# Kernel optimization log

Measured on AMD Instinct MI355X. Metric: run time of the kernel, lower is better.

The kernel has to match this reference:

```python
import jax, jax.numpy as jnp
import numpy as np

B, N, D = 4, 4096, 1024
H, S, R = 16, 256, 2           # heads, segment size, dilation rate
DH = D // H
LN_EPS = 1e-5


def _hilbert_perm(n_side):
    # perm[d] = linear index (y*side + x) of the d-th point on the Hilbert curve
    def d2xy(n, d):
        x = y = 0
        t = d
        s = 1
        while s < n:
            rx = 1 & (t // 2)
            ry = 1 & (t ^ rx)
            if ry == 0:
                if rx == 1:
                    x = s - 1 - x
                    y = s - 1 - y
                x, y = y, x
            x += s * rx
            y += s * ry
            t //= 4
            s *= 2
        return x, y
    perm = np.empty(n_side * n_side, dtype=np.int32)
    for d in range(n_side * n_side):
        xx, yy = d2xy(n_side, d)
        perm[d] = yy * n_side + xx
    return perm


def setup_inputs() -> dict:
    key = jax.random.key(0)
    ks = jax.random.split(key, 8)
    sc = 0.02
    return {
        "x": jax.random.normal(ks[0], (B, N, D), jnp.float32),
        "ln1_g": jnp.ones((D,), jnp.float32),
        "ln1_b": jnp.zeros((D,), jnp.float32),
        "w_qkv": jax.random.normal(ks[1], (D, 3 * D), jnp.float32) * sc,
        "b_qkv": jnp.zeros((3 * D,), jnp.float32),
        "w_o": jax.random.normal(ks[2], (D, D), jnp.float32) * sc,
        "b_o": jnp.zeros((D,), jnp.float32),
        "ln2_g": jnp.ones((D,), jnp.float32),
        "ln2_b": jnp.zeros((D,), jnp.float32),
        "w1": jax.random.normal(ks[3], (D, 4 * D), jnp.float32) * sc,
        "b1": jnp.zeros((4 * D,), jnp.float32),
        "w2": jax.random.normal(ks[4], (4 * D, D), jnp.float32) * sc,
        "b2": jnp.zeros((D,), jnp.float32),
        "hilbert_perm": jnp.asarray(_hilbert_perm(int(np.sqrt(N)))),
    }


def _layernorm(x, g, b):
    mu = jnp.mean(x, axis=-1, keepdims=True)
    var = jnp.mean(jnp.square(x - mu), axis=-1, keepdims=True)
    return (x - mu) * jax.lax.rsqrt(var + LN_EPS) * g + b


def _hilbert_dilated_attention(x, w_qkv, b_qkv, w_o, b_o, perm):
    b, n, d = x.shape
    nseg, sr = n // S, S // R
    xp = jnp.take(x, perm, axis=1)                    # Hilbert reorder
    qkv = xp @ w_qkv + b_qkv                          # [b,n,3d]
    q, k, v = jnp.split(qkv, 3, axis=-1)
    def seg(t):
        return t.reshape(b, nseg, S, H, DH)
    q, k, v = seg(q), seg(k), seg(v)
    # per-head dilation offset: head h attends positions (h % R) :: R in each segment
    offs = jnp.arange(H, dtype=jnp.int32) % R                        # [H]
    idx = offs[None, :] + R * jnp.arange(sr, dtype=jnp.int32)[:, None]  # [sr,H]
    idx_g = idx[None, None, :, :, None]                              # [1,1,sr,H,1]
    qd = jnp.take_along_axis(q, idx_g, axis=2)        # [b,nseg,sr,H,dh]
    kd = jnp.take_along_axis(k, idx_g, axis=2)
    vd = jnp.take_along_axis(v, idx_g, axis=2)
    scores = jnp.einsum('bgqhd,bgkhd->bghqk', qd, kd) / jnp.sqrt(jnp.asarray(DH, x.dtype))
    attn = jax.nn.softmax(scores, axis=-1)
    od = jnp.einsum('bghqk,bgkhd->bgqhd', attn, vd)   # [b,nseg,sr,H,dh]
    # scatter back into full segments; uncovered (head,pos) slots stay zero
    out = jnp.zeros((b, nseg, S, H, DH), x.dtype)
    out = out.at[:, :, idx, jnp.arange(H)[None, :], :].set(od)
    out = out.reshape(b, n, d) @ w_o + b_o
    inv = jnp.argsort(perm)
    return jnp.take(out, inv, axis=1)                 # inverse Hilbert reorder


def reference(x, ln1_g, ln1_b, w_qkv, b_qkv, w_o, b_o, ln2_g, ln2_b, w1, b1, w2, b2, hilbert_perm):
    h = _layernorm(x, ln1_g, ln1_b)
    h = _hilbert_dilated_attention(h, w_qkv, b_qkv, w_o, b_o, hilbert_perm)
    x = x + h
    h = _layernorm(x, ln2_g, ln2_b)
    h = jax.nn.gelu(h @ w1 + b1, approximate=False) @ w2 + b2
    return x + h
```

## Files before the change

kernel.cpp:

```cpp
#include <hip/hip_runtime.h>

typedef short bf16x8 __attribute__((ext_vector_type(8)));
typedef float f32x4 __attribute__((ext_vector_type(4)));
typedef unsigned short u16;

#define GLDS16(g, l) __builtin_amdgcn_global_load_lds( \
    (const __attribute__((address_space(1))) void*)(g), \
    (__attribute__((address_space(3))) void*)(l), 16, 0, 0)

__device__ __forceinline__ u16 f2b(float f) {
  unsigned u = __float_as_uint(f);
  u += 0x7fffu + ((u >> 16) & 1u);
  return (u16)(u >> 16);
}

__global__ __launch_bounds__(256)
void transpose_bf16(const float* __restrict__ w, u16* __restrict__ wt, int K, int N) {
  __shared__ float tile[32][33];
  const int n0 = blockIdx.x * 32, k0 = blockIdx.y * 32;
  const int tx = threadIdx.x & 31, ty = threadIdx.x >> 5;
#pragma unroll
  for (int i = 0; i < 4; ++i)
    tile[ty + i * 8][tx] = w[(size_t)(k0 + ty + i * 8) * N + n0 + tx];
  __syncthreads();
#pragma unroll
  for (int i = 0; i < 4; ++i)
    wt[(size_t)(n0 + ty + i * 8) * K + k0 + tx] = f2b(tile[tx][ty + i * 8]);
}

__global__ __launch_bounds__(256)
void ln_rows(const float* __restrict__ src, const float* __restrict__ gam,
             const float* __restrict__ bet, const int* __restrict__ perm,
             u16* __restrict__ dst) {
  const int orow = blockIdx.x;
  const int b = orow >> 12, j = orow & 4095;
  const int srow = perm ? ((b << 12) + perm[j]) : orow;
  const float4 v = ((const float4*)(src + (size_t)srow * 1024))[threadIdx.x];
  float s = v.x + v.y + v.z + v.w;
  float s2 = v.x * v.x + v.y * v.y + v.z * v.z + v.w * v.w;
#pragma unroll
  for (int d = 1; d < 64; d <<= 1) { s += __shfl_xor(s, d); s2 += __shfl_xor(s2, d); }
  __shared__ float rs[4], rs2[4];
  const int wave = threadIdx.x >> 6, lane = threadIdx.x & 63;
  if (lane == 0) { rs[wave] = s; rs2[wave] = s2; }
  __syncthreads();
  s = rs[0] + rs[1] + rs[2] + rs[3];
  s2 = rs2[0] + rs2[1] + rs2[2] + rs2[3];
  const float mu = s * (1.f / 1024.f);
  const float var = s2 * (1.f / 1024.f) - mu * mu;
  const float rstd = rsqrtf(var + 1e-5f);
  const int c = threadIdx.x * 4;
  const float4 gg = *(const float4*)(gam + c);
  const float4 bb = *(const float4*)(bet + c);
  const u16 o0 = f2b((v.x - mu) * rstd * gg.x + bb.x);
  const u16 o1 = f2b((v.y - mu) * rstd * gg.y + bb.y);
  const u16 o2 = f2b((v.z - mu) * rstd * gg.z + bb.z);
  const u16 o3 = f2b((v.w - mu) * rstd * gg.w + bb.w);
  const unsigned lo = (unsigned)o0 | ((unsigned)o1 << 16);
  const unsigned hi = (unsigned)o2 | ((unsigned)o3 << 16);
  *(uint2*)(dst + (size_t)orow * 1024 + c) = make_uint2(lo, hi);
}

template <int EPI>
__global__ __launch_bounds__(512, 2)
void gemm256(const u16* __restrict__ A, const u16* __restrict__ Bt,
             const float* __restrict__ bias, void* __restrict__ Cout,
             const float* __restrict__ resid, const int* __restrict__ perm,
             int M, int Nn, int K) {
  __shared__ u16 sm[65536];
  char* const smc = (char*)sm;
  const int tid = threadIdx.x;
  const int w = tid >> 6, lane = tid & 63;
  const int lr = lane & 15, lg = lane >> 4;
  const int wm = w >> 2, wn = w & 3;

  int wg = blockIdx.x;
  const int nwg = gridDim.x;
  if ((nwg & 7) == 0) { const int per = nwg >> 3; wg = (wg & 7) * per + (wg >> 3); }
  const int gx = M >> 8;
  const int m0 = (wg % gx) << 8, n0 = (wg / gx) << 8;

  const int srow = tid >> 3;
  const int scol = ((tid & 7) ^ (srow & 7)) << 3;
  const size_t aSrc = (size_t)(m0 + srow) * K + scol;
  const size_t bSrc = (size_t)(n0 + srow) * K + scol;
  char* const lWav = smc + w * 1024;

  const int slot0 = (lg ^ (lr & 7)) << 4;
  const int aRow = (wm * 128 + lr) * 128;
  const int bRow = (wn * 64 + lr) * 128 + 32768;

  const int NT = K >> 6;

#define STAGE_(d, mat, h, k0) do { \
    const u16* gp = ((mat) ? Bt : A) + ((mat) ? bSrc : aSrc) + (size_t)(h) * 128 * K + (k0); \
    char* lp = lWav + (d) * 65536 + (mat) * 32768 + (h) * 16384; \
    GLDS16(gp, lp); GLDS16(gp + (size_t)64 * K, lp + 8192); } while (0)

#define BAR_() do { asm volatile("" ::: "memory"); __builtin_amdgcn_s_barrier(); \
                    asm volatile("" ::: "memory"); } while (0)

  bf16x8 aLo[8], aHi[8], bb[8];

#define R_ALO(P) do { _Pragma("unroll") for (int mf = 0; mf < 4; ++mf) \
    _Pragma("unroll") for (int kk = 0; kk < 2; ++kk) \
      aLo[mf * 2 + kk] = *(const bf16x8*)((P) + mf * 2048 + (slot0 ^ (kk << 6))); } while (0)
#define R_AHI(P) do { _Pragma("unroll") for (int mf = 0; mf < 4; ++mf) \
    _Pragma("unroll") for (int kk = 0; kk < 2; ++kk) \
      aHi[mf * 2 + kk] = *(const bf16x8*)((P) + (4 + mf) * 2048 + (slot0 ^ (kk << 6))); } while (0)
#define R_B01(P) do { _Pragma("unroll") for (int nf = 0; nf < 2; ++nf) \
    _Pragma("unroll") for (int kk = 0; kk < 2; ++kk) \
      bb[nf * 2 + kk] = *(const bf16x8*)((P) + nf * 2048 + (slot0 ^ (kk << 6))); } while (0)
#define R_B23(P) do { _Pragma("unroll") for (int nf = 0; nf < 2; ++nf) \
    _Pragma("unroll") for (int kk = 0; kk < 2; ++kk) \
      bb[4 + nf * 2 + kk] = *(const bf16x8*)((P) + (2 + nf) * 2048 + (slot0 ^ (kk << 6))); } while (0)

#define C_QUAD(AARR, NB, MB) do { _Pragma("unroll") for (int mf = 0; mf < 4; ++mf) \
    _Pragma("unroll") for (int nf = 0; nf < 2; ++nf) \
    _Pragma("unroll") for (int kk = 0; kk < 2; ++kk) \
      acc[(MB) * 4 + mf][(NB) * 2 + nf] = __builtin_amdgcn_mfma_f32_16x16x32_bf16( \
          AARR[mf * 2 + kk], bb[(NB) * 4 + nf * 2 + kk], acc[(MB) * 4 + mf][(NB) * 2 + nf], 0, 0, 0); } while (0)

  STAGE_(0, 1, 0, 0); STAGE_(0, 1, 1, 0); STAGE_(0, 0, 0, 0); STAGE_(0, 0, 1, 0);
  if (NT > 1) {
    STAGE_(1, 1, 0, 64); STAGE_(1, 1, 1, 64); STAGE_(1, 0, 0, 64);
    asm volatile("s_waitcnt vmcnt(6)" ::: "memory");
  } else {
    asm volatile("s_waitcnt vmcnt(0)" ::: "memory");
  }
  BAR_();

  f32x4 acc[8][4] = {};
  R_ALO(smc + aRow);
  R_B01(smc + bRow);

  for (int t = 0; t < NT; ++t) {
    const int c = t & 1;
    const char* cA = smc + c * 65536 + aRow;
    const char* cB = smc + c * 65536 + bRow;
    const char* nA = smc + (c ^ 1) * 65536 + aRow;
    const char* nB = smc + (c ^ 1) * 65536 + bRow;

    R_B23(cB);
    if (t + 1 < NT) STAGE_(c ^ 1, 0, 1, (t + 1) << 6);
    BAR_();
    __builtin_amdgcn_s_setprio(1);
    C_QUAD(aLo, 0, 0);
    __builtin_amdgcn_s_setprio(0);
    BAR_();

    R_AHI(cA);
    if (t + 2 < NT) STAGE_(c, 1, 0, (t + 2) << 6);
    BAR_();
    __builtin_amdgcn_s_setprio(1);
    C_QUAD(aLo, 1, 0);
    __builtin_amdgcn_s_setprio(0);
    BAR_();

    if (t + 2 < NT) STAGE_(c, 1, 1, (t + 2) << 6);
    BAR_();
    __builtin_amdgcn_s_setprio(1);
    C_QUAD(aHi, 0, 1);
    __builtin_amdgcn_s_setprio(0);
    BAR_();

    if (t + 2 < NT) STAGE_(c, 0, 0, (t + 2) << 6);
    if (t < NT - 2) asm volatile("s_waitcnt vmcnt(6)" ::: "memory");
    else            asm volatile("s_waitcnt vmcnt(0)" ::: "memory");
    BAR_();
    if (t + 1 < NT) { R_ALO(nA); R_B01(nB); }
    __builtin_amdgcn_s_setprio(1);
    C_QUAD(aHi, 1, 1);
    __builtin_amdgcn_s_setprio(0);
    BAR_();
  }
#undef STAGE_
#undef BAR_
#undef R_ALO
#undef R_AHI
#undef R_B01
#undef R_B23
#undef C_QUAD

#pragma unroll
  for (int mf = 0; mf < 8; ++mf) {
#pragma unroll
    for (int nf = 0; nf < 4; ++nf) {
      const int col = n0 + wn * 64 + nf * 16 + lr;
      const float bia = bias[col];
#pragma unroll
      for (int r = 0; r < 4; ++r) {
        const int row = m0 + wm * 128 + mf * 16 + lg * 4 + r;
        float v = acc[mf][nf][r] + bia;
        if (EPI == 0) {
          ((u16*)Cout)[(size_t)row * Nn + col] = f2b(v);
        } else if (EPI == 1) {
          v = 0.5f * v * (1.f + erff(v * 0.70710678118654752f));
          ((u16*)Cout)[(size_t)row * Nn + col] = f2b(v);
        } else if (EPI == 2) {
          const int b = row >> 12, j = row & 4095;
          const size_t di = ((size_t)((b << 12) + perm[j])) * 1024 + col;
          ((float*)Cout)[di] = resid[di] + v;
        } else {
          const size_t di = (size_t)row * 1024 + col;
          ((float*)Cout)[di] = resid[di] + v;
        }
      }
    }
  }
}

__global__ __launch_bounds__(256, 2)
void attn_kernel(const u16* __restrict__ qkv, u16* __restrict__ outp) {
  const int blk = blockIdx.x;
  const int h = blk & 15, g = (blk >> 4) & 15, b = blk >> 8;
  const int tid = threadIdx.x, wave = tid >> 6, lane = tid & 63;
  const int lr = lane & 15, lg = lane >> 4;
  const int par = h & 1;

  __shared__ u16 lQ[128 * 64];
  __shared__ u16 lK[128 * 64];
  __shared__ u16 lVt[64 * 128];
  __shared__ u16 lP[4][32 * 128];

  const size_t rbase = (size_t)((b << 12) + (g << 8) + par);

#pragma unroll
  for (int i = 0; i < 4; ++i) {
    const int ou = i * 4096 + wave * 1024;
    const int o = ou + lane * 16;
    const int j = o >> 7, cb = o & 127;
    const u16* gq = qkv + (rbase + 2 * j) * 3072 + h * 64 + (cb >> 1);
    GLDS16(gq, (char*)lQ + ou);
    GLDS16(gq + 1024, (char*)lK + ou);
  }
#pragma unroll
  for (int i = 0; i < 4; ++i) {
    const int c = tid + i * 256;
    const int j = c >> 3, dc = c & 7;
    const uint4 vv = *(const uint4*)(qkv + (rbase + 2 * j) * 3072 + 2048 + h * 64 + dc * 8);
    const u16* pv = (const u16*)&vv;
#pragma unroll
    for (int e = 0; e < 8; ++e) lVt[(dc * 8 + e) * 128 + j] = pv[e];
  }
  __syncthreads();

  f32x4 sacc[2][8] = {};
#pragma unroll
  for (int kk = 0; kk < 2; ++kk) {
    bf16x8 aq[2], bk[8];
#pragma unroll
    for (int mf = 0; mf < 2; ++mf)
      aq[mf] = *(const bf16x8*)&lQ[(wave * 32 + mf * 16 + lr) * 64 + kk * 32 + lg * 8];
#pragma unroll
    for (int nf = 0; nf < 8; ++nf)
      bk[nf] = *(const bf16x8*)&lK[(nf * 16 + lr) * 64 + kk * 32 + lg * 8];
#pragma unroll
    for (int mf = 0; mf < 2; ++mf)
#pragma unroll
      for (int nf = 0; nf < 8; ++nf)
        sacc[mf][nf] = __builtin_amdgcn_mfma_f32_16x16x32_bf16(aq[mf], bk[nf], sacc[mf][nf], 0, 0, 0);
  }

#pragma unroll
  for (int mf = 0; mf < 2; ++mf) {
#pragma unroll
    for (int r = 0; r < 4; ++r) {
      float mx = -3e38f;
#pragma unroll
      for (int nf = 0; nf < 8; ++nf) mx = fmaxf(mx, sacc[mf][nf][r]);
#pragma unroll
      for (int d = 1; d < 16; d <<= 1) mx = fmaxf(mx, __shfl_xor(mx, d));
      float pv[8];
      float sum = 0.f;
#pragma unroll
      for (int nf = 0; nf < 8; ++nf) {
        pv[nf] = __expf((sacc[mf][nf][r] - mx) * 0.125f);
        sum += pv[nf];
      }
#pragma unroll
      for (int d = 1; d < 16; d <<= 1) sum += __shfl_xor(sum, d);
      const float inv = 1.f / sum;
      const int rrow = mf * 16 + lg * 4 + r;
#pragma unroll
      for (int nf = 0; nf < 8; ++nf)
        lP[wave][rrow * 128 + nf * 16 + lr] = f2b(pv[nf] * inv);
    }
  }
  __syncthreads();

  f32x4 oacc[2][4] = {};
#pragma unroll
  for (int kk = 0; kk < 4; ++kk) {
    bf16x8 ap[2], bv[4];
#pragma unroll
    for (int mf = 0; mf < 2; ++mf)
      ap[mf] = *(const bf16x8*)&lP[wave][(mf * 16 + lr) * 128 + kk * 32 + lg * 8];
#pragma unroll
    for (int nf = 0; nf < 4; ++nf)
      bv[nf] = *(const bf16x8*)&lVt[(nf * 16 + lr) * 128 + kk * 32 + lg * 8];
#pragma unroll
    for (int mf = 0; mf < 2; ++mf)
#pragma unroll
      for (int nf = 0; nf < 4; ++nf)
        oacc[mf][nf] = __builtin_amdgcn_mfma_f32_16x16x32_bf16(ap[mf], bv[nf], oacc[mf][nf], 0, 0, 0);
  }

  u16* obase = outp + ((size_t)((b << 12) + (g << 8))) * 1024 + h * 64;
#pragma unroll
  for (int mf = 0; mf < 2; ++mf)
#pragma unroll
    for (int nf = 0; nf < 4; ++nf)
#pragma unroll
      for (int r = 0; r < 4; ++r) {
        const int jq = wave * 32 + mf * 16 + lg * 4 + r;
        obase[(size_t)(par + 2 * jq) * 1024 + nf * 16 + lr] = f2b(oacc[mf][nf][r]);
      }
  const int jz = tid >> 1, hh = (tid & 1) * 32;
  u16* zp = obase + (size_t)((1 - par) + 2 * jz) * 1024 + hh;
  const uint4 z = make_uint4(0u, 0u, 0u, 0u);
#pragma unroll
  for (int i = 0; i < 4; ++i) ((uint4*)zp)[i] = z;
}

extern "C" void kernel_launch(void* const* d_in, const int* in_sizes, int n_in,
                              void* d_out, int out_size, void* d_ws, size_t ws_size,
                              hipStream_t stream) {
  const float* x    = (const float*)d_in[0];
  const float* ln1g = (const float*)d_in[1];
  const float* ln1b = (const float*)d_in[2];
  const float* wqkv = (const float*)d_in[3];
  const float* bqkv = (const float*)d_in[4];
  const float* wo   = (const float*)d_in[5];
  const float* bo   = (const float*)d_in[6];
  const float* ln2g = (const float*)d_in[7];
  const float* ln2b = (const float*)d_in[8];
  const float* w1   = (const float*)d_in[9];
  const float* b1   = (const float*)d_in[10];
  const float* w2   = (const float*)d_in[11];
  const float* b2   = (const float*)d_in[12];
  const int*   perm = (const int*)d_in[13];
  float* out = (float*)d_out;
  char* ws = (char*)d_ws;

  u16*  r0    = (u16*)ws;
  u16*  qkv   = (u16*)(ws + (32ull << 20));
  u16*  a1    = (u16*)(ws + (32ull << 20));
  float* x2   = (float*)(ws + (160ull << 20));
  u16*  wqkvT = (u16*)(ws + (224ull << 20));
  u16*  woT   = (u16*)(ws + (230ull << 20));
  u16*  w1T   = (u16*)(ws + (232ull << 20));
  u16*  w2T   = (u16*)(ws + (240ull << 20));

  transpose_bf16<<<dim3(3072 / 32, 1024 / 32), 256, 0, stream>>>(wqkv, wqkvT, 1024, 3072);
  transpose_bf16<<<dim3(1024 / 32, 1024 / 32), 256, 0, stream>>>(wo, woT, 1024, 1024);
  transpose_bf16<<<dim3(4096 / 32, 1024 / 32), 256, 0, stream>>>(w1, w1T, 1024, 4096);
  transpose_bf16<<<dim3(1024 / 32, 4096 / 32), 256, 0, stream>>>(w2, w2T, 4096, 1024);

  ln_rows<<<16384, 256, 0, stream>>>(x, ln1g, ln1b, perm, r0);
  gemm256<0><<<(16384 / 256) * (3072 / 256), 512, 0, stream>>>(r0, wqkvT, bqkv, qkv, nullptr, nullptr,
                                                               16384, 3072, 1024);
  attn_kernel<<<1024, 256, 0, stream>>>(qkv, r0);
  gemm256<2><<<(16384 / 256) * (1024 / 256), 512, 0, stream>>>(r0, woT, bo, x2, x, perm,
                                                               16384, 1024, 1024);
  ln_rows<<<16384, 256, 0, stream>>>(x2, ln2g, ln2b, nullptr, r0);
  gemm256<1><<<(16384 / 256) * (4096 / 256), 512, 0, stream>>>(r0, w1T, b1, a1, nullptr, nullptr,
                                                               16384, 4096, 1024);
  gemm256<3><<<(16384 / 256) * (1024 / 256), 512, 0, stream>>>(a1, w2T, b2, out, x2, nullptr,
                                                               16384, 1024, 4096);
}
```

Baseline: 612.1 us.

## Reorder GEMM main-loop LDS reads and quadrant order with explicit lgkmcnt waits

Restructures the 8-wave ping-pong GEMM inner loop. The A/B fragments are now read from LDS at the start of each iteration instead of being prefetched from the next buffer at the end. B is split into separate lo/hi register arrays and the quadrant order changes to (0,0),(0,1),(1,0),(1,1). The compiler memory-clobber barriers are replaced with raw s_barrier plus explicit lgkmcnt waits and sched_barrier fences, so LDS reads are placed precisely relative to the MFMA clusters. The goal is a tighter schedule and less register pressure. The trade-off is that the prefetch of the next tile's fragments no longer overlaps the last quadrant's MFMAs, and correctness now relies on the hand-placed waitcnts.

```diff
diff --git a/kernel.cpp b/kernel.cpp
--- a/kernel.cpp
+++ b/kernel.cpp
@@ -97,10 +97,7 @@
     char* lp = lWav + (d) * 65536 + (mat) * 32768 + (h) * 16384; \
     GLDS16(gp, lp); GLDS16(gp + (size_t)64 * K, lp + 8192); } while (0)
 
-#define BAR_() do { asm volatile("" ::: "memory"); __builtin_amdgcn_s_barrier(); \
-                    asm volatile("" ::: "memory"); } while (0)
-
-  bf16x8 aLo[8], aHi[8], bb[8];
+  bf16x8 aLo[8], aHi[8], bLo[4], bHi[4];
 
 #define R_ALO(P) do { _Pragma("unroll") for (int mf = 0; mf < 4; ++mf) \
     _Pragma("unroll") for (int kk = 0; kk < 2; ++kk) \
@@ -108,18 +105,21 @@
 #define R_AHI(P) do { _Pragma("unroll") for (int mf = 0; mf < 4; ++mf) \
     _Pragma("unroll") for (int kk = 0; kk < 2; ++kk) \
       aHi[mf * 2 + kk] = *(const bf16x8*)((P) + (4 + mf) * 2048 + (slot0 ^ (kk << 6))); } while (0)
-#define R_B01(P) do { _Pragma("unroll") for (int nf = 0; nf < 2; ++nf) \
-    _Pragma("unroll") for (int kk = 0; kk < 2; ++kk) \
-      bb[nf * 2 + kk] = *(const bf16x8*)((P) + nf * 2048 + (slot0 ^ (kk << 6))); } while (0)
-#define R_B23(P) do { _Pragma("unroll") for (int nf = 0; nf < 2; ++nf) \
-    _Pragma("unroll") for (int kk = 0; kk < 2; ++kk) \
-      bb[4 + nf * 2 + kk] = *(const bf16x8*)((P) + (2 + nf) * 2048 + (slot0 ^ (kk << 6))); } while (0)
-
-#define C_QUAD(AARR, NB, MB) do { _Pragma("unroll") for (int mf = 0; mf < 4; ++mf) \
+#define R_BLO(P) do { _Pragma("unroll") for (int nf = 0; nf < 2; ++nf) \
+    _Pragma("unroll") for (int kk = 0; kk < 2; ++kk) \
+      bLo[nf * 2 + kk] = *(const bf16x8*)((P) + nf * 2048 + (slot0 ^ (kk << 6))); } while (0)
+#define R_BHI(P) do { _Pragma("unroll") for (int nf = 0; nf < 2; ++nf) \
+    _Pragma("unroll") for (int kk = 0; kk < 2; ++kk) \
+      bHi[nf * 2 + kk] = *(const bf16x8*)((P) + (2 + nf) * 2048 + (slot0 ^ (kk << 6))); } while (0)
+
+#define QUAD_(AARR, BARR, MB, NB) do { _Pragma("unroll") for (int mf = 0; mf < 4; ++mf) \
     _Pragma("unroll") for (int nf = 0; nf < 2; ++nf) \
     _Pragma("unroll") for (int kk = 0; kk < 2; ++kk) \
       acc[(MB) * 4 + mf][(NB) * 2 + nf] = __builtin_amdgcn_mfma_f32_16x16x32_bf16( \
-          AARR[mf * 2 + kk], bb[(NB) * 4 + nf * 2 + kk], acc[(MB) * 4 + mf][(NB) * 2 + nf], 0, 0, 0); } while (0)
+          AARR[mf * 2 + kk], BARR[nf * 2 + kk], acc[(MB) * 4 + mf][(NB) * 2 + nf], 0, 0, 0); } while (0)
+
+#define LGKM0SB_() do { asm volatile("s_waitcnt lgkmcnt(0)" ::: "memory"); \
+                        __builtin_amdgcn_sched_barrier(0); } while (0)
 
   STAGE_(0, 1, 0, 0); STAGE_(0, 1, 1, 0); STAGE_(0, 0, 0, 0); STAGE_(0, 0, 1, 0);
   if (NT > 1) {
@@ -128,59 +128,60 @@
   } else {
     asm volatile("s_waitcnt vmcnt(0)" ::: "memory");
   }
-  BAR_();
+  __builtin_amdgcn_s_barrier();
 
   f32x4 acc[8][4] = {};
-  R_ALO(smc + aRow);
-  R_B01(smc + bRow);
 
   for (int t = 0; t < NT; ++t) {
     const int c = t & 1;
     const char* cA = smc + c * 65536 + aRow;
     const char* cB = smc + c * 65536 + bRow;
-    const char* nA = smc + (c ^ 1) * 65536 + aRow;
-    const char* nB = smc + (c ^ 1) * 65536 + bRow;
-
-    R_B23(cB);
+
+    R_ALO(cA); R_BLO(cB);
     if (t + 1 < NT) STAGE_(c ^ 1, 0, 1, (t + 1) << 6);
-    BAR_();
+    asm volatile("s_waitcnt lgkmcnt(8)" ::: "memory");
+    __builtin_amdgcn_s_barrier();
+    LGKM0SB_();
     __builtin_amdgcn_s_setprio(1);
-    C_QUAD(aLo, 0, 0);
+    QUAD_(aLo, bLo, 0, 0);
     __builtin_amdgcn_s_setprio(0);
-    BAR_();
+    __builtin_amdgcn_s_barrier();
+
+    R_BHI(cB);
+    if (t + 2 < NT) STAGE_(c, 1, 0, (t + 2) << 6);
+    __builtin_amdgcn_s_barrier();
+    LGKM0SB_();
+    __builtin_amdgcn_s_setprio(1);
+    QUAD_(aLo, bHi, 0, 1);
+    __builtin_amdgcn_s_setprio(0);
+    __builtin_amdgcn_s_barrier();
 
     R_AHI(cA);
-    if (t + 2 < NT) STAGE_(c, 1, 0, (t + 2) << 6);
-    BAR_();
+    if (t + 2 < NT) STAGE_(c, 1, 1, (t + 2) << 6);
+    __builtin_amdgcn_s_barrier();
+    LGKM0SB_();
     __builtin_amdgcn_s_setprio(1);
-    C_QUAD(aLo, 1, 0);
+    QUAD_(aHi, bLo, 1, 0);
     __builtin_amdgcn_s_setprio(0);
-    BAR_();
-
-    if (t + 2 < NT) STAGE_(c, 1, 1, (t + 2) << 6);
-    BAR_();
-    __builtin_amdgcn_s_setprio(1);
-    C_QUAD(aHi, 0, 1);
-    __builtin_amdgcn_s_setprio(0);
-    BAR_();
+    __builtin_amdgcn_s_barrier();
 
     if (t + 2 < NT) STAGE_(c, 0, 0, (t + 2) << 6);
     if (t < NT - 2) asm volatile("s_waitcnt vmcnt(6)" ::: "memory");
     else            asm volatile("s_waitcnt vmcnt(0)" ::: "memory");
-    BAR_();
-    if (t + 1 < NT) { R_ALO(nA); R_B01(nB); }
+    __builtin_amdgcn_s_barrier();
+    __builtin_amdgcn_sched_barrier(0);
     __builtin_amdgcn_s_setprio(1);
-    C_QUAD(aHi, 1, 1);
+    QUAD_(aHi, bHi, 1, 1);
     __builtin_amdgcn_s_setprio(0);
-    BAR_();
+    __builtin_amdgcn_s_barrier();
   }
 #undef STAGE_
-#undef BAR_
 #undef R_ALO
 #undef R_AHI
-#undef R_B01
-#undef R_B23
-#undef C_QUAD
+#undef R_BLO
+#undef R_BHI
+#undef QUAD_
+#undef LGKM0SB_
 
 #pragma unroll
   for (int mf = 0; mf < 8; ++mf) {
```

Measured after the change: 605.5 us. Within noise of the previous version (-1.1%).
